# Optimization experiments

Hardware: AMD Instinct MI355X
Metric: run time of the kernel (lower is better)

The kernel has to match this reference:

```python
import jax, jax.numpy as jnp
import numpy as np

B, L, DIM = 2, 2048, 2048
H, KV, HD = 32, 8, 64
N_REP = H // KV


def setup_inputs() -> dict:
    key = jax.random.key(0)
    ks = jax.random.split(key, 6)
    std = DIM ** -0.5
    std_o = (H * HD) ** -0.5 / np.sqrt(2 * 24)
    x = jax.random.normal(ks[0], (B, L, DIM), dtype=jnp.float32)
    # freqs_cis packs (cos, sin), each [L, head_dim//2]
    pos = jnp.arange(L, dtype=jnp.float32)[:, None]
    inv = 1.0 / (10000.0 ** (jnp.arange(0, HD, 2, dtype=jnp.float32) / HD))
    ang = pos * inv[None, :]
    freqs_cis = jnp.stack([jnp.cos(ang), jnp.sin(ang)], axis=0)
    wq = jax.random.normal(ks[1], (H * HD, DIM), dtype=jnp.float32) * std
    wk = jax.random.normal(ks[2], (KV * HD, DIM), dtype=jnp.float32) * std
    wv = jax.random.normal(ks[3], (KV * HD, DIM), dtype=jnp.float32) * std
    wo = jax.random.normal(ks[4], (DIM, H * HD), dtype=jnp.float32) * std_o
    return {"x": x, "freqs_cis": freqs_cis, "wq": wq, "wk": wk, "wv": wv, "wo": wo}


def _rope(t, cos, sin):
    # t: [B, L, h, HD]; interleaved (real, imag) pairs in last dim
    tr = t.reshape(*t.shape[:-1], HD // 2, 2)
    out_r = tr[..., 0] * cos - tr[..., 1] * sin
    out_i = tr[..., 0] * sin + tr[..., 1] * cos
    return jnp.stack([out_r, out_i], axis=-1).reshape(t.shape)


def reference(x, freqs_cis, wq, wk, wv, wo):
    Bb, Ll, _ = x.shape
    xq = (x @ wq.T).reshape(Bb, Ll, H, HD)
    xk = (x @ wk.T).reshape(Bb, Ll, KV, HD)
    xv = (x @ wv.T).reshape(Bb, Ll, KV, HD)
    cos = freqs_cis[0].reshape(1, Ll, 1, HD // 2)
    sin = freqs_cis[1].reshape(1, Ll, 1, HD // 2)
    xq = _rope(xq, cos, sin)
    xk = _rope(xk, cos, sin)
    # GQA: repeat_interleave kv heads to n_heads
    xk = jnp.repeat(xk, N_REP, axis=2)
    xv = jnp.repeat(xv, N_REP, axis=2)
    scale = 1.0 / jnp.sqrt(jnp.asarray(HD, x.dtype))
    scores = jnp.einsum('bihd,bjhd->bhij', xq, xk) * scale
    causal = jnp.tril(jnp.ones((Ll, Ll), dtype=bool))
    scores = jnp.where(causal[None, None], scores, jnp.finfo(scores.dtype).min)
    attn = jax.nn.softmax(scores, axis=-1)
    out = jnp.einsum('bhij,bjhd->bihd', attn, xv).reshape(Bb, Ll, H * HD)
    return out @ wo.T
```

## Files before the change

### kernel.cpp

```cpp
#include <hip/hip_runtime.h>
#include <stdint.h>

typedef __bf16 bf16;
typedef __attribute__((ext_vector_type(8))) __bf16 bf16x8;
typedef __attribute__((ext_vector_type(4))) __bf16 bf16x4;
typedef __attribute__((ext_vector_type(4))) short short4v;
typedef __attribute__((ext_vector_type(4))) float f32x4;

static constexpr int Bn = 2, Ln = 2048, DIMn = 2048, Hn = 32, KVn = 8, HDn = 64;
static constexpr int TS = 3072;

#if defined(__has_builtin)
#if __has_builtin(__builtin_amdgcn_exp2f)
#define EXP2(x) __builtin_amdgcn_exp2f(x)
#endif
#endif
#ifndef EXP2
#define EXP2(x) exp2f(x)
#endif

#define TO_LDS(p) ((__attribute__((address_space(3))) uint32_t*)(uintptr_t)(p))
#define TO_GLB(p) ((const __attribute__((address_space(1))) uint32_t*)(uintptr_t)(p))

__global__ void cast_all(const float* __restrict__ x, const float* __restrict__ wq,
                         const float* __restrict__ wk, const float* __restrict__ wv,
                         const float* __restrict__ wo, bf16* __restrict__ xb,
                         bf16* __restrict__ wqkvb, bf16* __restrict__ wob) {
    size_t i = (size_t)(blockIdx.x * blockDim.x + threadIdx.x) * 4;
    const float* src;
    bf16* dst;
    if (i < 8388608) {
        src = x + i; dst = xb + i;
    } else if (i < 8388608 + 6291456) {
        size_t j = i - 8388608;
        dst = wqkvb + j;
        if (j < 4194304)      src = wq + j;
        else if (j < 5242880) src = wk + (j - 4194304);
        else                  src = wv + (j - 5242880);
    } else {
        size_t j = i - 14680064;
        src = wo + j; dst = wob + j;
    }
    float4 v = *(const float4*)src;
    bf16 o[4] = {(bf16)v.x, (bf16)v.y, (bf16)v.z, (bf16)v.w};
    *(uint64_t*)dst = *(uint64_t*)o;
}

template <bool OUT_BF16>
__global__ __launch_bounds__(256) void gemm_bt(const bf16* __restrict__ A,
                                               const bf16* __restrict__ Bm,
                                               void* __restrict__ C,
                                               int M, int N, int K) {
    __shared__ bf16 sA[128 * 32];
    __shared__ bf16 sB[128 * 32];
    const int t    = threadIdx.x;
    const int wave = t >> 6, lane = t & 63;
    const int q4 = lane >> 4, l16 = lane & 15;
    const int bm = blockIdx.y * 128, bn = blockIdx.x * 128;
    const int wm = (wave >> 1) * 64, wn = (wave & 1) * 64;

    f32x4 acc[4][4] = {};

    const int srow = wave * 16 + (lane >> 2);
    const int scol = (lane & 3) * 8;
    const bf16* pa = A + (size_t)(bm + srow) * K + scol;
    const bf16* pb = Bm + (size_t)(bn + srow) * K + scol;
    bf16* la = &sA[wave * 16 * 32];
    bf16* lb = &sB[wave * 16 * 32];

    for (int k0 = 0; k0 < K; k0 += 32) {
#pragma unroll
        for (int p = 0; p < 2; ++p) {
            __builtin_amdgcn_global_load_lds(TO_GLB(pa + (size_t)p * 64 * K),
                                             TO_LDS(la + p * 64 * 32), 16, 0, 0);
            __builtin_amdgcn_global_load_lds(TO_GLB(pb + (size_t)p * 64 * K),
                                             TO_LDS(lb + p * 64 * 32), 16, 0, 0);
        }
        pa += 32; pb += 32;
        __syncthreads();
        bf16x8 af[4], bfr[4];
#pragma unroll
        for (int i = 0; i < 4; ++i) {
            af[i]  = *(const bf16x8*)(&sA[(wm + i * 16 + l16) * 32 + q4 * 8]);
            bfr[i] = *(const bf16x8*)(&sB[(wn + i * 16 + l16) * 32 + q4 * 8]);
        }
#pragma unroll
        for (int mi = 0; mi < 4; ++mi)
#pragma unroll
            for (int ni = 0; ni < 4; ++ni)
                acc[mi][ni] = __builtin_amdgcn_mfma_f32_16x16x32_bf16(af[mi], bfr[ni],
                                                                      acc[mi][ni], 0, 0, 0);
        __syncthreads();
    }

#pragma unroll
    for (int mi = 0; mi < 4; ++mi)
#pragma unroll
        for (int ni = 0; ni < 4; ++ni)
#pragma unroll
            for (int r = 0; r < 4; ++r) {
                size_t row = bm + wm + mi * 16 + q4 * 4 + r;
                size_t col = bn + wn + ni * 16 + l16;
                if (OUT_BF16)
                    ((bf16*)C)[row * N + col] = (bf16)acc[mi][ni][r];
                else
                    ((float*)C)[row * N + col] = acc[mi][ni][r];
            }
}

__global__ __launch_bounds__(256, 1) void attn_kernel(const bf16* __restrict__ QKV,
                                                      const float* __restrict__ fc,
                                                      bf16* __restrict__ O) {
    constexpr int LDK = 72;
    __shared__ bf16 sK[64 * LDK];
    __shared__ bf16 sV[64 * LDK];
    const int t    = threadIdx.x;
    const int wave = t >> 6, lane = t & 63;
    const int q4 = lane >> 4, l16 = lane & 15;
    const int pair = blockIdx.x, kvh = blockIdx.y, b = blockIdx.z;
    const int h = kvh * 4 + wave;
    constexpr float SC = 0.125f * 1.44269504088896340736f;

    const bf16* kb = QKV + (size_t)(b * Ln) * TS + 2048 + kvh * 64;
    const bf16* vb = kb + 512;
    const int krow = t >> 3;
    const int kc8  = (t & 7) * 8;
    const int kfrq = kc8 >> 1;
    const int vkey = t & 63, vhd0 = (t >> 6) * 16;

    for (int half = 0; half < 2; ++half) {
        const int qtile = half == 0 ? 31 - pair : pair;

        bf16x8 qf[4][2];
#pragma unroll
        for (int g = 0; g < 4; ++g) {
            int ql = qtile * 64 + g * 16 + l16;
            const bf16* qp = QKV + (size_t)(b * Ln + ql) * TS + h * 64;
#pragma unroll
            for (int hc = 0; hc < 2; ++hc) {
                bf16x8 raw = *(const bf16x8*)(qp + hc * 32 + q4 * 8);
                float4 c4 = *(const float4*)(fc + ql * 32 + hc * 16 + q4 * 4);
                float4 s4 = *(const float4*)(fc + 65536 + ql * 32 + hc * 16 + q4 * 4);
                bf16x8 o;
#pragma unroll
                for (int m = 0; m < 4; ++m) {
                    float cr = ((const float*)&c4)[m], sr = ((const float*)&s4)[m];
                    float x0 = (float)raw[2 * m], x1 = (float)raw[2 * m + 1];
                    o[2 * m]     = (bf16)((x0 * cr - x1 * sr) * SC);
                    o[2 * m + 1] = (bf16)((x0 * sr + x1 * cr) * SC);
                }
                qf[g][hc] = o;
            }
        }

        f32x4 o_acc[4][4] = {};
        float l_r[4] = {0.f, 0.f, 0.f, 0.f};

        bf16x8 kreg[2], vreg[2];
        float4 kc4[2], ks4[2];
        {
            const bf16* kp = kb;
            const bf16* vp = vb;
#pragma unroll
            for (int p = 0; p < 2; ++p) {
                int row = p * 32 + krow;
                kreg[p] = *(const bf16x8*)(kp + (size_t)row * TS + kc8);
                kc4[p] = *(const float4*)(fc + row * 32 + kfrq);
                ks4[p] = *(const float4*)(fc + 65536 + row * 32 + kfrq);
            }
            const bf16* v0 = vp + (size_t)vkey * TS + vhd0;
            vreg[0] = *(const bf16x8*)(v0);
            vreg[1] = *(const bf16x8*)(v0 + 8);
        }

        for (int kt = 0; kt <= qtile; ++kt) {
#pragma unroll
            for (int p = 0; p < 2; ++p) {
                int row = p * 32 + krow;
                bf16 out[8];
#pragma unroll
                for (int m = 0; m < 4; ++m) {
                    float cr = ((const float*)&kc4[p])[m], sr = ((const float*)&ks4[p])[m];
                    float x0 = (float)kreg[p][2 * m], x1 = (float)kreg[p][2 * m + 1];
                    out[2 * m]     = (bf16)(x0 * cr - x1 * sr);
                    out[2 * m + 1] = (bf16)(x0 * sr + x1 * cr);
                }
                *(float4*)(&sK[row * LDK + kc8]) = *(float4*)out;
            }
            {
                bf16 vv[16];
                *(bf16x8*)(vv)     = vreg[0];
                *(bf16x8*)(vv + 8) = vreg[1];
#pragma unroll
                for (int j = 0; j < 16; ++j) sV[(vhd0 + j) * LDK + vkey] = vv[j];
            }
            __syncthreads();

            if (kt < qtile) {
                const bf16* kp = kb + (size_t)(kt + 1) * 64 * TS;
                const bf16* vp = vb + (size_t)(kt + 1) * 64 * TS;
#pragma unroll
                for (int p = 0; p < 2; ++p) {
                    int row = p * 32 + krow;
                    kreg[p] = *(const bf16x8*)(kp + (size_t)row * TS + kc8);
                    int l = (kt + 1) * 64 + row;
                    kc4[p] = *(const float4*)(fc + l * 32 + kfrq);
                    ks4[p] = *(const float4*)(fc + 65536 + l * 32 + kfrq);
                }
                const bf16* v0 = vp + (size_t)vkey * TS + vhd0;
                vreg[0] = *(const bf16x8*)(v0);
                vreg[1] = *(const bf16x8*)(v0 + 8);
            }

            bf16x8 kf[4][2];
#pragma unroll
            for (int c = 0; c < 4; ++c)
#pragma unroll
                for (int hc = 0; hc < 2; ++hc)
                    kf[c][hc] = *(const bf16x8*)(&sK[(c * 16 + l16) * LDK + hc * 32 + q4 * 8]);
            short4v vf[4][4];
#pragma unroll
            for (int nc = 0; nc < 4; ++nc)
#pragma unroll
                for (int c = 0; c < 4; ++c)
                    vf[nc][c] = *(const short4v*)(&sV[(nc * 16 + l16) * LDK + c * 16 + q4 * 4]);

            const bool diag = (kt == qtile);
#pragma unroll
            for (int g = 0; g < 4; ++g) {
                f32x4 s[4];
#pragma unroll
                for (int c = 0; c < 4; ++c) {
                    f32x4 a = {};
                    a = __builtin_amdgcn_mfma_f32_16x16x32_bf16(kf[c][0], qf[g][0], a, 0, 0, 0);
                    a = __builtin_amdgcn_mfma_f32_16x16x32_bf16(kf[c][1], qf[g][1], a, 0, 0, 0);
                    s[c] = a;
                }
                int qrow = qtile * 64 + g * 16 + l16;
                float lsum = 0.f;
                short4v pb4[4];
#pragma unroll
                for (int c = 0; c < 4; ++c)
#pragma unroll
                    for (int r = 0; r < 4; ++r) {
                        float p = EXP2(s[c][r] - 12.f);
                        if (diag && (kt * 64 + c * 16 + q4 * 4 + r > qrow)) p = 0.f;
                        lsum += p;
                        bf16 ph = (bf16)p;
                        pb4[c][r] = *(const short*)&ph;
                    }
                l_r[g] += lsum;
#pragma unroll
                for (int nc = 0; nc < 4; ++nc)
#pragma unroll
                    for (int c = 0; c < 4; ++c)
                        o_acc[g][nc] = __builtin_amdgcn_mfma_f32_16x16x16bf16_1k(
                            vf[nc][c], pb4[c], o_acc[g][nc], 0, 0, 0);
            }
            __syncthreads();
        }

#pragma unroll
        for (int g = 0; g < 4; ++g) {
            float l = l_r[g];
            l += __shfl_xor(l, 16, 64);
            l += __shfl_xor(l, 32, 64);
            float inv = 1.f / l;
            int qrow = qtile * 64 + g * 16 + l16;
            bf16* op = O + (size_t)(b * Ln + qrow) * (Hn * HDn) + h * 64;
#pragma unroll
            for (int nc = 0; nc < 4; ++nc) {
                bf16x4 o;
#pragma unroll
                for (int r = 0; r < 4; ++r) o[r] = (bf16)(o_acc[g][nc][r] * inv);
                *(bf16x4*)(op + nc * 16 + q4 * 4) = o;
            }
        }
    }
}

extern "C" void kernel_launch(void* const* d_in, const int* in_sizes, int n_in,
                              void* d_out, int out_size, void* d_ws, size_t ws_size,
                              hipStream_t stream) {
    const float* x  = (const float*)d_in[0];
    const float* fc = (const float*)d_in[1];
    const float* wq = (const float*)d_in[2];
    const float* wk = (const float*)d_in[3];
    const float* wv = (const float*)d_in[4];
    const float* wo = (const float*)d_in[5];
    float* out = (float*)d_out;

    const size_t T = (size_t)Bn * Ln;
    char* p = (char*)d_ws;
    bf16* xb    = (bf16*)p; p += T * DIMn * 2;
    bf16* wqkvb = (bf16*)p; p += (size_t)TS * DIMn * 2;
    bf16* wob   = (bf16*)p; p += (size_t)DIMn * Hn * HDn * 2;
    bf16* qkv   = (bf16*)p; p += T * TS * 2;
    bf16* ao    = (bf16*)p; p += T * Hn * HDn * 2;

    cast_all<<<dim3(18432), dim3(256), 0, stream>>>(x, wq, wk, wv, wo, xb, wqkvb, wob);

    gemm_bt<true><<<dim3(TS / 128, 32), dim3(256), 0, stream>>>(xb, wqkvb, qkv, 4096, TS, 2048);

    attn_kernel<<<dim3(16, KVn, Bn), dim3(256), 0, stream>>>(qkv, fc, ao);

    gemm_bt<false><<<dim3(16, 32), dim3(256), 0, stream>>>(ao, wob, out, 4096, 2048, 2048);
}
```

Baseline: 327.2 us.

## Split attention key columns across two wave groups and precompute K RoPE

Doubles the attention block to 512 threads. Each head's 64-key tile is split between two waves, each doing half the QK and PV MFMAs. Partial outputs and row sums are combined through a new LDS buffer before normalisation. K RoPE moves into a separate in-place kernel that runs before attention, so K tiles are copied to LDS without per-tile trig math. This targets the low occupancy of a 256-block grid of 256-thread blocks, at the cost of more LDS, an extra launch, and a combine step with extra barriers.

Measured after the change: 307.5 us. 1.06x faster.

```diff
diff --git a/kernel.cpp b/kernel.cpp
--- a/kernel.cpp
+++ b/kernel.cpp
@@ -46,6 +46,20 @@
     *(uint64_t*)dst = *(uint64_t*)o;
 }
 
+__global__ void rope_k(bf16* __restrict__ qkv, const float* __restrict__ fc) {
+    int idx = blockIdx.x * blockDim.x + threadIdx.x;
+    int i   = idx & 31;
+    int kvh = (idx >> 5) & 7;
+    int bl  = idx >> 8;
+    int l   = bl & (Ln - 1);
+    size_t base = (size_t)bl * TS + 2048 + kvh * 64 + 2 * i;
+    float cr = fc[l * 32 + i];
+    float sr = fc[65536 + l * 32 + i];
+    float x0 = (float)qkv[base], x1 = (float)qkv[base + 1];
+    qkv[base]     = (bf16)(x0 * cr - x1 * sr);
+    qkv[base + 1] = (bf16)(x0 * sr + x1 * cr);
+}
+
 template <bool OUT_BF16>
 __global__ __launch_bounds__(256) void gemm_bt(const bf16* __restrict__ A,
                                                const bf16* __restrict__ Bm,
@@ -108,25 +122,28 @@
             }
 }
 
-__global__ __launch_bounds__(256, 1) void attn_kernel(const bf16* __restrict__ QKV,
+__global__ __launch_bounds__(512, 1) void attn_kernel(const bf16* __restrict__ QKV,
                                                       const float* __restrict__ fc,
                                                       bf16* __restrict__ O) {
     constexpr int LDK = 72;
     __shared__ bf16 sK[64 * LDK];
     __shared__ bf16 sV[64 * LDK];
+    __shared__ float sComb[4][64][68];
+    __shared__ float sL[4][64][4];
     const int t    = threadIdx.x;
     const int wave = t >> 6, lane = t & 63;
     const int q4 = lane >> 4, l16 = lane & 15;
+    const int hidx = wave & 3, kh = wave >> 2;
     const int pair = blockIdx.x, kvh = blockIdx.y, b = blockIdx.z;
-    const int h = kvh * 4 + wave;
+    const int h = kvh * 4 + hidx;
+    const int c0 = kh * 2;
     constexpr float SC = 0.125f * 1.44269504088896340736f;
 
     const bf16* kb = QKV + (size_t)(b * Ln) * TS + 2048 + kvh * 64;
     const bf16* vb = kb + 512;
     const int krow = t >> 3;
     const int kc8  = (t & 7) * 8;
-    const int kfrq = kc8 >> 1;
-    const int vkey = t & 63, vhd0 = (t >> 6) * 16;
+    const int vkey = t & 63, vhd0 = (t >> 6) * 8;
 
     for (int half = 0; half < 2; ++half) {
         const int qtile = half == 0 ? 31 - pair : pair;
@@ -156,126 +173,108 @@
         f32x4 o_acc[4][4] = {};
         float l_r[4] = {0.f, 0.f, 0.f, 0.f};
 
-        bf16x8 kreg[2], vreg[2];
-        float4 kc4[2], ks4[2];
-        {
-            const bf16* kp = kb;
-            const bf16* vp = vb;
-#pragma unroll
-            for (int p = 0; p < 2; ++p) {
-                int row = p * 32 + krow;
-                kreg[p] = *(const bf16x8*)(kp + (size_t)row * TS + kc8);
-                kc4[p] = *(const float4*)(fc + row * 32 + kfrq);
-                ks4[p] = *(const float4*)(fc + 65536 + row * 32 + kfrq);
-            }
-            const bf16* v0 = vp + (size_t)vkey * TS + vhd0;
-            vreg[0] = *(const bf16x8*)(v0);
-            vreg[1] = *(const bf16x8*)(v0 + 8);
-        }
+        bf16x8 kreg = *(const bf16x8*)(kb + (size_t)krow * TS + kc8);
+        bf16x8 vreg = *(const bf16x8*)(vb + (size_t)vkey * TS + vhd0);
 
         for (int kt = 0; kt <= qtile; ++kt) {
-#pragma unroll
-            for (int p = 0; p < 2; ++p) {
-                int row = p * 32 + krow;
-                bf16 out[8];
-#pragma unroll
-                for (int m = 0; m < 4; ++m) {
-                    float cr = ((const float*)&kc4[p])[m], sr = ((const float*)&ks4[p])[m];
-                    float x0 = (float)kreg[p][2 * m], x1 = (float)kreg[p][2 * m + 1];
-                    out[2 * m]     = (bf16)(x0 * cr - x1 * sr);
-                    out[2 * m + 1] = (bf16)(x0 * sr + x1 * cr);
-                }
-                *(float4*)(&sK[row * LDK + kc8]) = *(float4*)out;
-            }
+            *(float4*)(&sK[krow * LDK + kc8]) = *(float4*)&kreg;
             {
-                bf16 vv[16];
-                *(bf16x8*)(vv)     = vreg[0];
-                *(bf16x8*)(vv + 8) = vreg[1];
-#pragma unroll
-                for (int j = 0; j < 16; ++j) sV[(vhd0 + j) * LDK + vkey] = vv[j];
+                bf16 vv[8];
+                *(bf16x8*)vv = vreg;
+#pragma unroll
+                for (int j = 0; j < 8; ++j) sV[(vhd0 + j) * LDK + vkey] = vv[j];
             }
             __syncthreads();
 
             if (kt < qtile) {
-                const bf16* kp = kb + (size_t)(kt + 1) * 64 * TS;
-                const bf16* vp = vb + (size_t)(kt + 1) * 64 * TS;
-#pragma unroll
-                for (int p = 0; p < 2; ++p) {
-                    int row = p * 32 + krow;
-                    kreg[p] = *(const bf16x8*)(kp + (size_t)row * TS + kc8);
-                    int l = (kt + 1) * 64 + row;
-                    kc4[p] = *(const float4*)(fc + l * 32 + kfrq);
-                    ks4[p] = *(const float4*)(fc + 65536 + l * 32 + kfrq);
-                }
-                const bf16* v0 = vp + (size_t)vkey * TS + vhd0;
-                vreg[0] = *(const bf16x8*)(v0);
-                vreg[1] = *(const bf16x8*)(v0 + 8);
-            }
-
-            bf16x8 kf[4][2];
-#pragma unroll
-            for (int c = 0; c < 4; ++c)
+                kreg = *(const bf16x8*)(kb + (size_t)((kt + 1) * 64 + krow) * TS + kc8);
+                vreg = *(const bf16x8*)(vb + (size_t)((kt + 1) * 64 + vkey) * TS + vhd0);
+            }
+
+            bf16x8 kf[2][2];
+#pragma unroll
+            for (int ci = 0; ci < 2; ++ci)
 #pragma unroll
                 for (int hc = 0; hc < 2; ++hc)
-                    kf[c][hc] = *(const bf16x8*)(&sK[(c * 16 + l16) * LDK + hc * 32 + q4 * 8]);
-            short4v vf[4][4];
+                    kf[ci][hc] = *(const bf16x8*)(&sK[((c0 + ci) * 16 + l16) * LDK + hc * 32 + q4 * 8]);
+            short4v vf[4][2];
 #pragma unroll
             for (int nc = 0; nc < 4; ++nc)
 #pragma unroll
-                for (int c = 0; c < 4; ++c)
-                    vf[nc][c] = *(const short4v*)(&sV[(nc * 16 + l16) * LDK + c * 16 + q4 * 4]);
+                for (int ci = 0; ci < 2; ++ci)
+                    vf[nc][ci] = *(const short4v*)(&sV[(nc * 16 + l16) * LDK + (c0 + ci) * 16 + q4 * 4]);
 
             const bool diag = (kt == qtile);
 #pragma unroll
             for (int g = 0; g < 4; ++g) {
-                f32x4 s[4];
-#pragma unroll
-                for (int c = 0; c < 4; ++c) {
+                f32x4 s[2];
+#pragma unroll
+                for (int ci = 0; ci < 2; ++ci) {
                     f32x4 a = {};
-                    a = __builtin_amdgcn_mfma_f32_16x16x32_bf16(kf[c][0], qf[g][0], a, 0, 0, 0);
-                    a = __builtin_amdgcn_mfma_f32_16x16x32_bf16(kf[c][1], qf[g][1], a, 0, 0, 0);
-                    s[c] = a;
+                    a = __builtin_amdgcn_mfma_f32_16x16x32_bf16(kf[ci][0], qf[g][0], a, 0, 0, 0);
+                    a = __builtin_amdgcn_mfma_f32_16x16x32_bf16(kf[ci][1], qf[g][1], a, 0, 0, 0);
+                    s[ci] = a;
                 }
                 int qrow = qtile * 64 + g * 16 + l16;
                 float lsum = 0.f;
-                short4v pb4[4];
-#pragma unroll
-                for (int c = 0; c < 4; ++c)
+                short4v pb4[2];
+#pragma unroll
+                for (int ci = 0; ci < 2; ++ci)
 #pragma unroll
                     for (int r = 0; r < 4; ++r) {
-                        float p = EXP2(s[c][r] - 12.f);
-                        if (diag && (kt * 64 + c * 16 + q4 * 4 + r > qrow)) p = 0.f;
+                        float p = EXP2(s[ci][r] - 12.f);
+                        if (diag && (kt * 64 + (c0 + ci) * 16 + q4 * 4 + r > qrow)) p = 0.f;
                         lsum += p;
                         bf16 ph = (bf16)p;
-                        pb4[c][r] = *(const short*)&ph;
+                        pb4[ci][r] = *(const short*)&ph;
                     }
                 l_r[g] += lsum;
 #pragma unroll
                 for (int nc = 0; nc < 4; ++nc)
 #pragma unroll
-                    for (int c = 0; c < 4; ++c)
+                    for (int ci = 0; ci < 2; ++ci)
                         o_acc[g][nc] = __builtin_amdgcn_mfma_f32_16x16x16bf16_1k(
-                            vf[nc][c], pb4[c], o_acc[g][nc], 0, 0, 0);
+                            vf[nc][ci], pb4[ci], o_acc[g][nc], 0, 0, 0);
             }
             __syncthreads();
         }
 
-#pragma unroll
-        for (int g = 0; g < 4; ++g) {
-            float l = l_r[g];
-            l += __shfl_xor(l, 16, 64);
-            l += __shfl_xor(l, 32, 64);
-            float inv = 1.f / l;
-            int qrow = qtile * 64 + g * 16 + l16;
-            bf16* op = O + (size_t)(b * Ln + qrow) * (Hn * HDn) + h * 64;
-#pragma unroll
-            for (int nc = 0; nc < 4; ++nc) {
-                bf16x4 o;
-#pragma unroll
-                for (int r = 0; r < 4; ++r) o[r] = (bf16)(o_acc[g][nc][r] * inv);
-                *(bf16x4*)(op + nc * 16 + q4 * 4) = o;
-            }
-        }
+        if (kh) {
+#pragma unroll
+            for (int g = 0; g < 4; ++g) {
+#pragma unroll
+                for (int nc = 0; nc < 4; ++nc)
+                    *(f32x4*)(&sComb[hidx][lane][g * 16 + nc * 4]) = o_acc[g][nc];
+                sL[hidx][lane][g] = l_r[g];
+            }
+        }
+        __syncthreads();
+        if (!kh) {
+#pragma unroll
+            for (int g = 0; g < 4; ++g) {
+                l_r[g] += sL[hidx][lane][g];
+#pragma unroll
+                for (int nc = 0; nc < 4; ++nc)
+                    o_acc[g][nc] += *(const f32x4*)(&sComb[hidx][lane][g * 16 + nc * 4]);
+            }
+#pragma unroll
+            for (int g = 0; g < 4; ++g) {
+                float l = l_r[g];
+                l += __shfl_xor(l, 16, 64);
+                l += __shfl_xor(l, 32, 64);
+                float inv = 1.f / l;
+                int qrow = qtile * 64 + g * 16 + l16;
+                bf16* op = O + (size_t)(b * Ln + qrow) * (Hn * HDn) + h * 64;
+#pragma unroll
+                for (int nc = 0; nc < 4; ++nc) {
+                    bf16x4 o;
+#pragma unroll
+                    for (int r = 0; r < 4; ++r) o[r] = (bf16)(o_acc[g][nc][r] * inv);
+                    *(bf16x4*)(op + nc * 16 + q4 * 4) = o;
+                }
+            }
+        }
+        __syncthreads();
     }
 }
 
@@ -302,7 +301,9 @@
 
     gemm_bt<true><<<dim3(TS / 128, 32), dim3(256), 0, stream>>>(xb, wqkvb, qkv, 4096, TS, 2048);
 
-    attn_kernel<<<dim3(16, KVn, Bn), dim3(256), 0, stream>>>(qkv, fc, ao);
+    rope_k<<<dim3(4096), dim3(256), 0, stream>>>(qkv, fc);
+
+    attn_kernel<<<dim3(16, KVn, Bn), dim3(512), 0, stream>>>(qkv, fc, ao);
 
     gemm_bt<false><<<dim3(16, 32), dim3(256), 0, stream>>>(ao, wob, out, 4096, 2048, 2048);
 }
```

## Precompute K RoPE and V transpose, run attention as single-wave blocks without LDS

Applied to the files above, without the earlier changes.

Key RoPE now runs in a separate in-place pass over the QKV buffer, and V is transposed into a head-major layout by its own kernel. The attention kernel changes from 4-wave blocks that each handle a pair of q-tiles to 64-thread blocks, one per head and q-tile. Each block reads K and the transposed V straight from global memory into MFMA fragments, with no LDS staging and no barriers. This increases block count and removes synchronisation, at the cost of two extra launches. It also drops the K/V sharing across the 4 GQA heads through LDS, so global and L2 traffic goes up. Causal load balance now relies on the scheduler instead of the q-tile pairing.

Result: slower. 423.6 us (+29.5%).

```diff
diff --git a/kernel.cpp b/kernel.cpp
--- a/kernel.cpp
+++ b/kernel.cpp
@@ -46,6 +46,43 @@
     *(uint64_t*)dst = *(uint64_t*)o;
 }
 
+__global__ void rope_k(bf16* __restrict__ qkv, const float* __restrict__ fc) {
+    int idx = blockIdx.x * blockDim.x + threadIdx.x;
+    int i   = idx & 31;
+    int kvh = (idx >> 5) & 7;
+    int bl  = idx >> 8;
+    int l   = bl & (Ln - 1);
+    size_t base = (size_t)bl * TS + 2048 + kvh * 64 + 2 * i;
+    float cr = fc[l * 32 + i];
+    float sr = fc[65536 + l * 32 + i];
+    float x0 = (float)qkv[base], x1 = (float)qkv[base + 1];
+    qkv[base]     = (bf16)(x0 * cr - x1 * sr);
+    qkv[base + 1] = (bf16)(x0 * sr + x1 * cr);
+}
+
+__global__ __launch_bounds__(256) void transpose_v(const bf16* __restrict__ qkv,
+                                                   bf16* __restrict__ Vt) {
+    __shared__ bf16 sT[64][72];
+    const int t = threadIdx.x;
+    const int lt = blockIdx.x, kvh = blockIdx.y, b = blockIdx.z;
+    const bf16* vp = qkv + (size_t)(b * Ln + lt * 64) * TS + 2560 + kvh * 64;
+    {
+        int key = t & 63, hd0 = (t >> 6) * 16;
+        *(bf16x8*)(&sT[key][hd0])     = *(const bf16x8*)(vp + (size_t)key * TS + hd0);
+        *(bf16x8*)(&sT[key][hd0 + 8]) = *(const bf16x8*)(vp + (size_t)key * TS + hd0 + 8);
+    }
+    __syncthreads();
+    {
+        int hd = t >> 2, kcol = (t & 3) * 16;
+        bf16 v[16];
+#pragma unroll
+        for (int j = 0; j < 16; ++j) v[j] = sT[kcol + j][hd];
+        bf16* dst = Vt + ((size_t)(b * KVn + kvh) * 64 + hd) * Ln + lt * 64 + kcol;
+        *(bf16x8*)(dst)     = *(bf16x8*)(v);
+        *(bf16x8*)(dst + 8) = *(bf16x8*)(v + 8);
+    }
+}
+
 template <bool OUT_BF16>
 __global__ __launch_bounds__(256) void gemm_bt(const bf16* __restrict__ A,
                                                const bf16* __restrict__ Bm,
@@ -108,173 +145,120 @@
             }
 }
 
-__global__ __launch_bounds__(256, 1) void attn_kernel(const bf16* __restrict__ QKV,
-                                                      const float* __restrict__ fc,
-                                                      bf16* __restrict__ O) {
-    constexpr int LDK = 72;
-    __shared__ bf16 sK[64 * LDK];
-    __shared__ bf16 sV[64 * LDK];
-    const int t    = threadIdx.x;
-    const int wave = t >> 6, lane = t & 63;
+__global__ __launch_bounds__(64, 2) void attn_kernel(const bf16* __restrict__ QKV,
+                                                     const bf16* __restrict__ Vt,
+                                                     const float* __restrict__ fc,
+                                                     bf16* __restrict__ O) {
+    const int lane = threadIdx.x;
     const int q4 = lane >> 4, l16 = lane & 15;
-    const int pair = blockIdx.x, kvh = blockIdx.y, b = blockIdx.z;
-    const int h = kvh * 4 + wave;
+    const int qt   = 31 - (blockIdx.x & 31);
+    const int hidx = blockIdx.x >> 5;
+    const int kvh = blockIdx.y, b = blockIdx.z;
+    const int h = kvh * 4 + hidx;
     constexpr float SC = 0.125f * 1.44269504088896340736f;
 
+    bf16x8 qf[4][2];
+#pragma unroll
+    for (int g = 0; g < 4; ++g) {
+        int ql = qt * 64 + g * 16 + l16;
+        const bf16* qp = QKV + (size_t)(b * Ln + ql) * TS + h * 64;
+#pragma unroll
+        for (int hc = 0; hc < 2; ++hc) {
+            bf16x8 raw = *(const bf16x8*)(qp + hc * 32 + q4 * 8);
+            float4 c4 = *(const float4*)(fc + ql * 32 + hc * 16 + q4 * 4);
+            float4 s4 = *(const float4*)(fc + 65536 + ql * 32 + hc * 16 + q4 * 4);
+            bf16x8 o;
+#pragma unroll
+            for (int m = 0; m < 4; ++m) {
+                float cr = ((const float*)&c4)[m], sr = ((const float*)&s4)[m];
+                float x0 = (float)raw[2 * m], x1 = (float)raw[2 * m + 1];
+                o[2 * m]     = (bf16)((x0 * cr - x1 * sr) * SC);
+                o[2 * m + 1] = (bf16)((x0 * sr + x1 * cr) * SC);
+            }
+            qf[g][hc] = o;
+        }
+    }
+
     const bf16* kb = QKV + (size_t)(b * Ln) * TS + 2048 + kvh * 64;
-    const bf16* vb = kb + 512;
-    const int krow = t >> 3;
-    const int kc8  = (t & 7) * 8;
-    const int kfrq = kc8 >> 1;
-    const int vkey = t & 63, vhd0 = (t >> 6) * 16;
-
-    for (int half = 0; half < 2; ++half) {
-        const int qtile = half == 0 ? 31 - pair : pair;
-
-        bf16x8 qf[4][2];
+    const bf16* vt = Vt + (size_t)(b * KVn + kvh) * 64 * Ln;
+
+    f32x4 o_acc[4][4] = {};
+    float l_r[4] = {0.f, 0.f, 0.f, 0.f};
+
+    bf16x8 kf[4][2];
+#pragma unroll
+    for (int c = 0; c < 4; ++c)
+#pragma unroll
+        for (int hc = 0; hc < 2; ++hc)
+            kf[c][hc] = *(const bf16x8*)(kb + (size_t)(c * 16 + l16) * TS + hc * 32 + q4 * 8);
+
+    for (int kt = 0; kt <= qt; ++kt) {
+        short4v vf[4][4];
+#pragma unroll
+        for (int nc = 0; nc < 4; ++nc)
+#pragma unroll
+            for (int c = 0; c < 4; ++c)
+                vf[nc][c] = *(const short4v*)(vt + (size_t)(nc * 16 + l16) * Ln +
+                                              kt * 64 + c * 16 + q4 * 4);
+
+        const bool diag = (kt == qt);
 #pragma unroll
         for (int g = 0; g < 4; ++g) {
-            int ql = qtile * 64 + g * 16 + l16;
-            const bf16* qp = QKV + (size_t)(b * Ln + ql) * TS + h * 64;
-#pragma unroll
-            for (int hc = 0; hc < 2; ++hc) {
-                bf16x8 raw = *(const bf16x8*)(qp + hc * 32 + q4 * 8);
-                float4 c4 = *(const float4*)(fc + ql * 32 + hc * 16 + q4 * 4);
-                float4 s4 = *(const float4*)(fc + 65536 + ql * 32 + hc * 16 + q4 * 4);
-                bf16x8 o;
-#pragma unroll
-                for (int m = 0; m < 4; ++m) {
-                    float cr = ((const float*)&c4)[m], sr = ((const float*)&s4)[m];
-                    float x0 = (float)raw[2 * m], x1 = (float)raw[2 * m + 1];
-                    o[2 * m]     = (bf16)((x0 * cr - x1 * sr) * SC);
-                    o[2 * m + 1] = (bf16)((x0 * sr + x1 * cr) * SC);
+            f32x4 s[4];
+#pragma unroll
+            for (int c = 0; c < 4; ++c) {
+                f32x4 a = {};
+                a = __builtin_amdgcn_mfma_f32_16x16x32_bf16(kf[c][0], qf[g][0], a, 0, 0, 0);
+                a = __builtin_amdgcn_mfma_f32_16x16x32_bf16(kf[c][1], qf[g][1], a, 0, 0, 0);
+                s[c] = a;
+            }
+            int qrow = qt * 64 + g * 16 + l16;
+            float lsum = 0.f;
+            short4v pb4[4];
+#pragma unroll
+            for (int c = 0; c < 4; ++c)
+#pragma unroll
+                for (int r = 0; r < 4; ++r) {
+                    float p = EXP2(s[c][r] - 12.f);
+                    if (diag && (kt * 64 + c * 16 + q4 * 4 + r > qrow)) p = 0.f;
+                    lsum += p;
+                    bf16 ph = (bf16)p;
+                    pb4[c][r] = *(const short*)&ph;
                 }
-                qf[g][hc] = o;
-            }
-        }
-
-        f32x4 o_acc[4][4] = {};
-        float l_r[4] = {0.f, 0.f, 0.f, 0.f};
-
-        bf16x8 kreg[2], vreg[2];
-        float4 kc4[2], ks4[2];
-        {
-            const bf16* kp = kb;
-            const bf16* vp = vb;
-#pragma unroll
-            for (int p = 0; p < 2; ++p) {
-                int row = p * 32 + krow;
-                kreg[p] = *(const bf16x8*)(kp + (size_t)row * TS + kc8);
-                kc4[p] = *(const float4*)(fc + row * 32 + kfrq);
-                ks4[p] = *(const float4*)(fc + 65536 + row * 32 + kfrq);
-            }
-            const bf16* v0 = vp + (size_t)vkey * TS + vhd0;
-            vreg[0] = *(const bf16x8*)(v0);
-            vreg[1] = *(const bf16x8*)(v0 + 8);
-        }
-
-        for (int kt = 0; kt <= qtile; ++kt) {
-#pragma unroll
-            for (int p = 0; p < 2; ++p) {
-                int row = p * 32 + krow;
-                bf16 out[8];
-#pragma unroll
-                for (int m = 0; m < 4; ++m) {
-                    float cr = ((const float*)&kc4[p])[m], sr = ((const float*)&ks4[p])[m];
-                    float x0 = (float)kreg[p][2 * m], x1 = (float)kreg[p][2 * m + 1];
-                    out[2 * m]     = (bf16)(x0 * cr - x1 * sr);
-                    out[2 * m + 1] = (bf16)(x0 * sr + x1 * cr);
-                }
-                *(float4*)(&sK[row * LDK + kc8]) = *(float4*)out;
-            }
-            {
-                bf16 vv[16];
-                *(bf16x8*)(vv)     = vreg[0];
-                *(bf16x8*)(vv + 8) = vreg[1];
-#pragma unroll
-                for (int j = 0; j < 16; ++j) sV[(vhd0 + j) * LDK + vkey] = vv[j];
-            }
-            __syncthreads();
-
-            if (kt < qtile) {
-                const bf16* kp = kb + (size_t)(kt + 1) * 64 * TS;
-                const bf16* vp = vb + (size_t)(kt + 1) * 64 * TS;
-#pragma unroll
-                for (int p = 0; p < 2; ++p) {
-                    int row = p * 32 + krow;
-                    kreg[p] = *(const bf16x8*)(kp + (size_t)row * TS + kc8);
-                    int l = (kt + 1) * 64 + row;
-                    kc4[p] = *(const float4*)(fc + l * 32 + kfrq);
-                    ks4[p] = *(const float4*)(fc + 65536 + l * 32 + kfrq);
-                }
-                const bf16* v0 = vp + (size_t)vkey * TS + vhd0;
-                vreg[0] = *(const bf16x8*)(v0);
-                vreg[1] = *(const bf16x8*)(v0 + 8);
-            }
-
-            bf16x8 kf[4][2];
+            l_r[g] += lsum;
+#pragma unroll
+            for (int nc = 0; nc < 4; ++nc)
+#pragma unroll
+                for (int c = 0; c < 4; ++c)
+                    o_acc[g][nc] = __builtin_amdgcn_mfma_f32_16x16x16bf16_1k(
+                        vf[nc][c], pb4[c], o_acc[g][nc], 0, 0, 0);
+        }
+
+        if (kt < qt) {
+            const bf16* kp = kb + (size_t)(kt + 1) * 64 * TS;
 #pragma unroll
             for (int c = 0; c < 4; ++c)
 #pragma unroll
                 for (int hc = 0; hc < 2; ++hc)
-                    kf[c][hc] = *(const bf16x8*)(&sK[(c * 16 + l16) * LDK + hc * 32 + q4 * 8]);
-            short4v vf[4][4];
-#pragma unroll
-            for (int nc = 0; nc < 4; ++nc)
-#pragma unroll
-                for (int c = 0; c < 4; ++c)
-                    vf[nc][c] = *(const short4v*)(&sV[(nc * 16 + l16) * LDK + c * 16 + q4 * 4]);
-
-            const bool diag = (kt == qtile);
-#pragma unroll
-            for (int g = 0; g < 4; ++g) {
-                f32x4 s[4];
-#pragma unroll
-                for (int c = 0; c < 4; ++c) {
-                    f32x4 a = {};
-                    a = __builtin_amdgcn_mfma_f32_16x16x32_bf16(kf[c][0], qf[g][0], a, 0, 0, 0);
-                    a = __builtin_amdgcn_mfma_f32_16x16x32_bf16(kf[c][1], qf[g][1], a, 0, 0, 0);
-                    s[c] = a;
-                }
-                int qrow = qtile * 64 + g * 16 + l16;
-                float lsum = 0.f;
-                short4v pb4[4];
-#pragma unroll
-                for (int c = 0; c < 4; ++c)
-#pragma unroll
-                    for (int r = 0; r < 4; ++r) {
-                        float p = EXP2(s[c][r] - 12.f);
-                        if (diag && (kt * 64 + c * 16 + q4 * 4 + r > qrow)) p = 0.f;
-                        lsum += p;
-                        bf16 ph = (bf16)p;
-                        pb4[c][r] = *(const short*)&ph;
-                    }
-                l_r[g] += lsum;
-#pragma unroll
-                for (int nc = 0; nc < 4; ++nc)
-#pragma unroll
-                    for (int c = 0; c < 4; ++c)
-                        o_acc[g][nc] = __builtin_amdgcn_mfma_f32_16x16x16bf16_1k(
-                            vf[nc][c], pb4[c], o_acc[g][nc], 0, 0, 0);
-            }
-            __syncthreads();
-        }
-
-#pragma unroll
-        for (int g = 0; g < 4; ++g) {
-            float l = l_r[g];
-            l += __shfl_xor(l, 16, 64);
-            l += __shfl_xor(l, 32, 64);
-            float inv = 1.f / l;
-            int qrow = qtile * 64 + g * 16 + l16;
-            bf16* op = O + (size_t)(b * Ln + qrow) * (Hn * HDn) + h * 64;
-#pragma unroll
-            for (int nc = 0; nc < 4; ++nc) {
-                bf16x4 o;
-#pragma unroll
-                for (int r = 0; r < 4; ++r) o[r] = (bf16)(o_acc[g][nc][r] * inv);
-                *(bf16x4*)(op + nc * 16 + q4 * 4) = o;
-            }
+                    kf[c][hc] = *(const bf16x8*)(kp + (size_t)(c * 16 + l16) * TS +
+                                                 hc * 32 + q4 * 8);
+        }
+    }
+
+#pragma unroll
+    for (int g = 0; g < 4; ++g) {
+        float l = l_r[g];
+        l += __shfl_xor(l, 16, 64);
+        l += __shfl_xor(l, 32, 64);
+        float inv = 1.f / l;
+        int qrow = qt * 64 + g * 16 + l16;
+        bf16* op = O + (size_t)(b * Ln + qrow) * (Hn * HDn) + h * 64;
+#pragma unroll
+        for (int nc = 0; nc < 4; ++nc) {
+            bf16x4 o;
+#pragma unroll
+            for (int r = 0; r < 4; ++r) o[r] = (bf16)(o_acc[g][nc][r] * inv);
+            *(bf16x4*)(op + nc * 16 + q4 * 4) = o;
         }
     }
 }
@@ -297,12 +281,16 @@
     bf16* wob   = (bf16*)p; p += (size_t)DIMn * Hn * HDn * 2;
     bf16* qkv   = (bf16*)p; p += T * TS * 2;
     bf16* ao    = (bf16*)p; p += T * Hn * HDn * 2;
+    bf16* vtb   = (bf16*)p; p += (size_t)Bn * KVn * 64 * Ln * 2;
 
     cast_all<<<dim3(18432), dim3(256), 0, stream>>>(x, wq, wk, wv, wo, xb, wqkvb, wob);
 
     gemm_bt<true><<<dim3(TS / 128, 32), dim3(256), 0, stream>>>(xb, wqkvb, qkv, 4096, TS, 2048);
 
-    attn_kernel<<<dim3(16, KVn, Bn), dim3(256), 0, stream>>>(qkv, fc, ao);
+    rope_k<<<dim3(4096), dim3(256), 0, stream>>>(qkv, fc);
+    transpose_v<<<dim3(Ln / 64, KVn, Bn), dim3(256), 0, stream>>>(qkv, vtb);
+
+    attn_kernel<<<dim3(128, KVn, Bn), dim3(64), 0, stream>>>(qkv, vtb, fc, ao);
 
     gemm_bt<false><<<dim3(16, 32), dim3(256), 0, stream>>>(ao, wob, out, 4096, 2048, 2048);
 }
```

## Precompute K RoPE in separate pass and split attention heads across more blocks

Applied to the files above, without the earlier changes.

Adds a standalone kernel that applies RoPE to K in place once, so the attention loop no longer reloads cos/sin and re-rotates every K tile for each query tile. The attention grid is reorganized: each block now handles two heads, with waves split over head and query-row halves, which doubles the block count to 512 and allows two blocks per CU. The cost is an extra kernel launch plus a read-modify-write pass over K, and K/V tiles are now staged into LDS twice as many times in total because each block covers only two heads.

Result: faster. 304.1 us (-7.1%).

```diff
diff --git a/kernel.cpp b/kernel.cpp
--- a/kernel.cpp
+++ b/kernel.cpp
@@ -46,6 +46,20 @@
     *(uint64_t*)dst = *(uint64_t*)o;
 }
 
+__global__ void rope_k(bf16* __restrict__ qkv, const float* __restrict__ fc) {
+    int idx = blockIdx.x * blockDim.x + threadIdx.x;
+    int i   = idx & 31;
+    int kvh = (idx >> 5) & 7;
+    int bl  = idx >> 8;
+    int l   = bl & (Ln - 1);
+    size_t base = (size_t)bl * TS + 2048 + kvh * 64 + 2 * i;
+    float cr = fc[l * 32 + i];
+    float sr = fc[65536 + l * 32 + i];
+    float x0 = (float)qkv[base], x1 = (float)qkv[base + 1];
+    qkv[base]     = (bf16)(x0 * cr - x1 * sr);
+    qkv[base + 1] = (bf16)(x0 * sr + x1 * cr);
+}
+
 template <bool OUT_BF16>
 __global__ __launch_bounds__(256) void gemm_bt(const bf16* __restrict__ A,
                                                const bf16* __restrict__ Bm,
@@ -108,7 +122,7 @@
             }
 }
 
-__global__ __launch_bounds__(256, 1) void attn_kernel(const bf16* __restrict__ QKV,
+__global__ __launch_bounds__(256, 2) void attn_kernel(const bf16* __restrict__ QKV,
                                                       const float* __restrict__ fc,
                                                       bf16* __restrict__ O) {
     constexpr int LDK = 72;
@@ -117,24 +131,25 @@
     const int t    = threadIdx.x;
     const int wave = t >> 6, lane = t & 63;
     const int q4 = lane >> 4, l16 = lane & 15;
-    const int pair = blockIdx.x, kvh = blockIdx.y, b = blockIdx.z;
-    const int h = kvh * 4 + wave;
+    const int hidx = wave & 1, qh = wave >> 1;
+    const int L = blockIdx.x;
+    const int pair = L & 15, hp = (L >> 4) & 1, kvh = (L >> 5) & 7, b = L >> 8;
+    const int h = kvh * 4 + hp * 2 + hidx;
     constexpr float SC = 0.125f * 1.44269504088896340736f;
 
     const bf16* kb = QKV + (size_t)(b * Ln) * TS + 2048 + kvh * 64;
     const bf16* vb = kb + 512;
     const int krow = t >> 3;
     const int kc8  = (t & 7) * 8;
-    const int kfrq = kc8 >> 1;
     const int vkey = t & 63, vhd0 = (t >> 6) * 16;
 
     for (int half = 0; half < 2; ++half) {
         const int qtile = half == 0 ? 31 - pair : pair;
 
-        bf16x8 qf[4][2];
-#pragma unroll
-        for (int g = 0; g < 4; ++g) {
-            int ql = qtile * 64 + g * 16 + l16;
+        bf16x8 qf[2][2];
+#pragma unroll
+        for (int g2 = 0; g2 < 2; ++g2) {
+            int ql = qtile * 64 + (qh * 2 + g2) * 16 + l16;
             const bf16* qp = QKV + (size_t)(b * Ln + ql) * TS + h * 64;
 #pragma unroll
             for (int hc = 0; hc < 2; ++hc) {
@@ -149,44 +164,27 @@
                     o[2 * m]     = (bf16)((x0 * cr - x1 * sr) * SC);
                     o[2 * m + 1] = (bf16)((x0 * sr + x1 * cr) * SC);
                 }
-                qf[g][hc] = o;
-            }
-        }
-
-        f32x4 o_acc[4][4] = {};
-        float l_r[4] = {0.f, 0.f, 0.f, 0.f};
+                qf[g2][hc] = o;
+            }
+        }
+
+        f32x4 o_acc[2][4] = {};
+        float l_r[2] = {0.f, 0.f};
 
         bf16x8 kreg[2], vreg[2];
-        float4 kc4[2], ks4[2];
+#pragma unroll
+        for (int p = 0; p < 2; ++p)
+            kreg[p] = *(const bf16x8*)(kb + (size_t)(p * 32 + krow) * TS + kc8);
         {
-            const bf16* kp = kb;
-            const bf16* vp = vb;
-#pragma unroll
-            for (int p = 0; p < 2; ++p) {
-                int row = p * 32 + krow;
-                kreg[p] = *(const bf16x8*)(kp + (size_t)row * TS + kc8);
-                kc4[p] = *(const float4*)(fc + row * 32 + kfrq);
-                ks4[p] = *(const float4*)(fc + 65536 + row * 32 + kfrq);
-            }
-            const bf16* v0 = vp + (size_t)vkey * TS + vhd0;
+            const bf16* v0 = vb + (size_t)vkey * TS + vhd0;
             vreg[0] = *(const bf16x8*)(v0);
             vreg[1] = *(const bf16x8*)(v0 + 8);
         }
 
         for (int kt = 0; kt <= qtile; ++kt) {
 #pragma unroll
-            for (int p = 0; p < 2; ++p) {
-                int row = p * 32 + krow;
-                bf16 out[8];
-#pragma unroll
-                for (int m = 0; m < 4; ++m) {
-                    float cr = ((const float*)&kc4[p])[m], sr = ((const float*)&ks4[p])[m];
-                    float x0 = (float)kreg[p][2 * m], x1 = (float)kreg[p][2 * m + 1];
-                    out[2 * m]     = (bf16)(x0 * cr - x1 * sr);
-                    out[2 * m + 1] = (bf16)(x0 * sr + x1 * cr);
-                }
-                *(float4*)(&sK[row * LDK + kc8]) = *(float4*)out;
-            }
+            for (int p = 0; p < 2; ++p)
+                *(float4*)(&sK[(p * 32 + krow) * LDK + kc8]) = *(float4*)&kreg[p];
             {
                 bf16 vv[16];
                 *(bf16x8*)(vv)     = vreg[0];
@@ -197,17 +195,10 @@
             __syncthreads();
 
             if (kt < qtile) {
-                const bf16* kp = kb + (size_t)(kt + 1) * 64 * TS;
-                const bf16* vp = vb + (size_t)(kt + 1) * 64 * TS;
-#pragma unroll
-                for (int p = 0; p < 2; ++p) {
-                    int row = p * 32 + krow;
-                    kreg[p] = *(const bf16x8*)(kp + (size_t)row * TS + kc8);
-                    int l = (kt + 1) * 64 + row;
-                    kc4[p] = *(const float4*)(fc + l * 32 + kfrq);
-                    ks4[p] = *(const float4*)(fc + 65536 + l * 32 + kfrq);
-                }
-                const bf16* v0 = vp + (size_t)vkey * TS + vhd0;
+#pragma unroll
+                for (int p = 0; p < 2; ++p)
+                    kreg[p] = *(const bf16x8*)(kb + (size_t)((kt + 1) * 64 + p * 32 + krow) * TS + kc8);
+                const bf16* v0 = vb + (size_t)((kt + 1) * 64 + vkey) * TS + vhd0;
                 vreg[0] = *(const bf16x8*)(v0);
                 vreg[1] = *(const bf16x8*)(v0 + 8);
             }
@@ -227,16 +218,16 @@
 
             const bool diag = (kt == qtile);
 #pragma unroll
-            for (int g = 0; g < 4; ++g) {
+            for (int g2 = 0; g2 < 2; ++g2) {
                 f32x4 s[4];
 #pragma unroll
                 for (int c = 0; c < 4; ++c) {
                     f32x4 a = {};
-                    a = __builtin_amdgcn_mfma_f32_16x16x32_bf16(kf[c][0], qf[g][0], a, 0, 0, 0);
-                    a = __builtin_amdgcn_mfma_f32_16x16x32_bf16(kf[c][1], qf[g][1], a, 0, 0, 0);
+                    a = __builtin_amdgcn_mfma_f32_16x16x32_bf16(kf[c][0], qf[g2][0], a, 0, 0, 0);
+                    a = __builtin_amdgcn_mfma_f32_16x16x32_bf16(kf[c][1], qf[g2][1], a, 0, 0, 0);
                     s[c] = a;
                 }
-                int qrow = qtile * 64 + g * 16 + l16;
+                int qrow = qtile * 64 + (qh * 2 + g2) * 16 + l16;
                 float lsum = 0.f;
                 short4v pb4[4];
 #pragma unroll
@@ -249,30 +240,30 @@
                         bf16 ph = (bf16)p;
                         pb4[c][r] = *(const short*)&ph;
                     }
-                l_r[g] += lsum;
+                l_r[g2] += lsum;
 #pragma unroll
                 for (int nc = 0; nc < 4; ++nc)
 #pragma unroll
                     for (int c = 0; c < 4; ++c)
-                        o_acc[g][nc] = __builtin_amdgcn_mfma_f32_16x16x16bf16_1k(
-                            vf[nc][c], pb4[c], o_acc[g][nc], 0, 0, 0);
+                        o_acc[g2][nc] = __builtin_amdgcn_mfma_f32_16x16x16bf16_1k(
+                            vf[nc][c], pb4[c], o_acc[g2][nc], 0, 0, 0);
             }
             __syncthreads();
         }
 
 #pragma unroll
-        for (int g = 0; g < 4; ++g) {
-            float l = l_r[g];
+        for (int g2 = 0; g2 < 2; ++g2) {
+            float l = l_r[g2];
             l += __shfl_xor(l, 16, 64);
             l += __shfl_xor(l, 32, 64);
             float inv = 1.f / l;
-            int qrow = qtile * 64 + g * 16 + l16;
+            int qrow = qtile * 64 + (qh * 2 + g2) * 16 + l16;
             bf16* op = O + (size_t)(b * Ln + qrow) * (Hn * HDn) + h * 64;
 #pragma unroll
             for (int nc = 0; nc < 4; ++nc) {
                 bf16x4 o;
 #pragma unroll
-                for (int r = 0; r < 4; ++r) o[r] = (bf16)(o_acc[g][nc][r] * inv);
+                for (int r = 0; r < 4; ++r) o[r] = (bf16)(o_acc[g2][nc][r] * inv);
                 *(bf16x4*)(op + nc * 16 + q4 * 4) = o;
             }
         }
@@ -302,7 +293,9 @@
 
     gemm_bt<true><<<dim3(TS / 128, 32), dim3(256), 0, stream>>>(xb, wqkvb, qkv, 4096, TS, 2048);
 
-    attn_kernel<<<dim3(16, KVn, Bn), dim3(256), 0, stream>>>(qkv, fc, ao);
+    rope_k<<<dim3(4096), dim3(256), 0, stream>>>(qkv, fc);
+
+    attn_kernel<<<dim3(512), dim3(256), 0, stream>>>(qkv, fc, ao);
 
     gemm_bt<false><<<dim3(16, 32), dim3(256), 0, stream>>>(ao, wob, out, 4096, 2048, 2048);
 }
```
